# Performance work log

Measured on AMD Instinct MI355X. Metric: run time of the kernel, lower is better.

The kernel has to match this reference:

```python
import jax, jax.numpy as jnp
import numpy as np

NN_SIZE = 16  # nn_size from __init__


def _knn_idx(points_ref, k):
    """Brute-force KNN of points_ref against itself (replaces faiss_knn).
    Returns (B, N, k) neighbor indices, self point excluded."""
    sq = jnp.sum(points_ref * points_ref, axis=-1)  # (B, N)
    # squared pairwise distances (B, N, N)
    d2 = sq[:, :, None] + sq[:, None, :] - 2.0 * jnp.einsum(
        'bnd,bmd->bnm', points_ref, points_ref)
    _, idx = jax.lax.top_k(-d2, k + 1)  # nearest first; idx[...,0] is self
    return idx[:, :, 1:]


def _edge_lengths(pts, knn_idx):
    """Gather neighbor coords and compute edge lengths (B, N, K)."""
    group = jax.vmap(lambda p, i: p[i])(pts, knn_idx)  # (B, N, K, D)
    return jnp.linalg.norm(group - pts[:, :, None, :], axis=-1)


def setup_inputs() -> dict:
    key = jax.random.key(0)
    k1, k2 = jax.random.split(key)
    B, N, D = 4, 8192, 3
    points_ref = jax.random.normal(k1, (B, N, D), dtype=jnp.float32)
    # pred points: perturbed ref so the loss is non-degenerate
    points = points_ref + 0.01 * jax.random.normal(k2, (B, N, D), dtype=jnp.float32)
    return {"points_ref": points_ref, "points": points}


def reference(points_ref, points):
    # faiss KNN is non-differentiable -> stop_gradient on the index search
    knn_idx = _knn_idx(jax.lax.stop_gradient(points_ref), NN_SIZE)  # (B,N,K)
    dist_ref = _edge_lengths(points_ref, knn_idx)  # (B, N, K)
    dist = _edge_lengths(points, knn_idx)          # (B, N, K)
    # metric = torch.nn.L1Loss() (mean reduction)
    return jnp.mean(jnp.abs(dist_ref - dist))
```

## Files before the change

### kernel.cpp

```cpp
#include <hip/hip_runtime.h>
#include <math.h>

#define BATCH 4
#define NPTS  8192
#define KNN   16
#define KK    17
#define NQ    (BATCH*NPTS)
#define JMASK 0x1FFFu
#define EMASK 0xFFFFE000u
#define TOTAL_EDGES (BATCH*NPTS*KNN)

#define GC    32
#define GLO   (-4.5f)
#define GINV  (32.0f/9.0f)
#define NCELL (GC*GC*GC)

#define NG    128
#define GSZ   64

#define QPB   16
#define BLOCK 256
#define GRIDQ (NQ/QPB)
#define WIN   64
#define CAP   21

__device__ __forceinline__ int cell_coord(float x) {
    int c = (int)floorf((x - GLO) * GINV);
    return min(GC - 1, max(0, c));
}
__device__ __forceinline__ unsigned spread5(unsigned v) {
    v &= 31u;
    v = (v | (v << 8)) & 0x100Fu;
    v = (v | (v << 4)) & 0x10C3u;
    v = (v | (v << 2)) & 0x1249u;
    return v;
}
__device__ __forceinline__ unsigned morton_id(float x, float y, float z) {
    return spread5((unsigned)cell_coord(x)) | (spread5((unsigned)cell_coord(y)) << 1)
         | (spread5((unsigned)cell_coord(z)) << 2);
}
__device__ __forceinline__ unsigned mkkey(const float4 p, float xi, float yi,
                                          float zi, float sqi, unsigned j) {
    const float e  = fmaf(p.x, xi, fmaf(p.y, yi, p.z * zi)) + p.w;
    const float d2 = e + sqi;
    return (__float_as_uint(d2) & EMASK) | j;
}
__device__ __forceinline__ void ins17(unsigned (&a)[KK], unsigned key) {
    #pragma unroll
    for (int k = KK - 1; k >= 1; --k) a[k] = min(a[k], max(a[k - 1], key));
    a[0] = min(a[0], key);
}
template<int RL>
__device__ __forceinline__ unsigned merge_tau(const unsigned (*s_key)[BLOCK], int t) {
    const int mq = t & (QPB - 1), half = (t >> 4) & 1;
    unsigned m[KK];
    #pragma unroll
    for (int k = 0; k < KK; ++k) m[k] = 0xFFFFFFFFu;
    for (int s = 8 * half; s < 8 * half + 8; ++s) {
        const int col = mq + s * QPB;
        for (int k = 0; k < RL; ++k) {
            const unsigned c = s_key[k][col];
            if (c >= m[KK - 1]) break;
            ins17(m, c);
        }
    }
    unsigned tau = 0;
    #pragma unroll
    for (int k = 0; k < KK; ++k) {
        const unsigned bk = (unsigned)__shfl_xor((int)m[KK - 1 - k], 16, 64);
        tau = max(tau, min(m[k], bk));
    }
    return tau;
}

__global__ void pel_hist(const float* __restrict__ pref, unsigned* __restrict__ hist,
                         float* __restrict__ acc, unsigned* __restrict__ bcnt) {
    const int idx = blockIdx.x * 256 + threadIdx.x;
    if (idx == 0) { acc[0] = 0.0f; bcnt[0] = 0u; }
    const int b = idx >> 13;
    const unsigned mid = morton_id(pref[3*idx], pref[3*idx+1], pref[3*idx+2]);
    atomicAdd(&hist[b * NCELL + mid], 1u);
}
__global__ __launch_bounds__(1024)
void pel_scan(const unsigned* __restrict__ hist, unsigned* __restrict__ off) {
    __shared__ unsigned s[1024];
    const unsigned* h = hist + blockIdx.x * NCELL;
    unsigned*       o = off  + blockIdx.x * NCELL;
    const int t = threadIdx.x;
    unsigned v[32], tot = 0;
    #pragma unroll
    for (int k = 0; k < 32; ++k) { v[k] = h[t * 32 + k]; tot += v[k]; }
    s[t] = tot;
    __syncthreads();
    for (int d = 1; d < 1024; d <<= 1) {
        const unsigned add = (t >= d) ? s[t - d] : 0u;
        __syncthreads();
        s[t] += add;
        __syncthreads();
    }
    unsigned run = s[t] - tot;
    #pragma unroll
    for (int k = 0; k < 32; ++k) { o[t * 32 + k] = run; run += v[k]; }
}
__global__ void pel_scatter(const float* __restrict__ pref, const float* __restrict__ pts,
                            unsigned* __restrict__ off,
                            float4* __restrict__ p4r, float4* __restrict__ p4p) {
    const int idx = blockIdx.x * 256 + threadIdx.x;
    const int b = idx >> 13;
    const float x = pref[3*idx], y = pref[3*idx+1], z = pref[3*idx+2];
    const unsigned mid = morton_id(x, y, z);
    const unsigned pos = atomicAdd(&off[b * NCELL + mid], 1u);
    p4r[b * NPTS + pos] = make_float4(-2.f*x, -2.f*y, -2.f*z, fmaf(x, x, fmaf(y, y, z*z)));
    const float px = pts[3*idx], py = pts[3*idx+1], pz = pts[3*idx+2];
    p4p[b * NPTS + pos] = make_float4(-2.f*px, -2.f*py, -2.f*pz,
                                      fmaf(px, px, fmaf(py, py, pz*pz)));
}
__global__ __launch_bounds__(256)
void pel_gstat(const float4* __restrict__ P4r, float4* __restrict__ gball) {
    const int wv = threadIdx.x >> 6, lane = threadIdx.x & 63;
    const int gid = blockIdx.x * 4 + wv;
    const int b = gid >> 7, g = gid & (NG - 1);
    const float4 p = P4r[b * NPTS + g * GSZ + lane];
    const float x = -0.5f * p.x, y = -0.5f * p.y, z = -0.5f * p.z;
    float mnx = x, mxx = x, mny = y, mxy = y, mnz = z, mxz = z;
    #pragma unroll
    for (int m = 1; m <= 32; m <<= 1) {
        mnx = fminf(mnx, __shfl_xor(mnx, m, 64)); mxx = fmaxf(mxx, __shfl_xor(mxx, m, 64));
        mny = fminf(mny, __shfl_xor(mny, m, 64)); mxy = fmaxf(mxy, __shfl_xor(mxy, m, 64));
        mnz = fminf(mnz, __shfl_xor(mnz, m, 64)); mxz = fmaxf(mxz, __shfl_xor(mxz, m, 64));
    }
    const float cx = 0.5f * (mnx + mxx), cy = 0.5f * (mny + mxy), cz = 0.5f * (mnz + mxz);
    float d = sqrtf((x-cx)*(x-cx) + (y-cy)*(y-cy) + (z-cz)*(z-cz));
    #pragma unroll
    for (int m = 1; m <= 32; m <<= 1) d = fmaxf(d, __shfl_xor(d, m, 64));
    if (lane == 0) gball[gid] = make_float4(cx, cy, cz, d);
}

__global__ __launch_bounds__(BLOCK, 8)
void pel_query(const float4* __restrict__ P4r, const float4* __restrict__ P4p,
               const float4* __restrict__ gball,
               float* __restrict__ acc_ws, unsigned* __restrict__ bcnt,
               float* __restrict__ out)
{
    __shared__ unsigned s_key[CAP][BLOCK];
    __shared__ unsigned s_tau[QPB];
    __shared__ unsigned short s_glist[NG];
    __shared__ float s_grp[4];
    __shared__ int s_ng;
    __shared__ float s_part[BLOCK / 64];

    const int t  = threadIdx.x;
    const int lq = t & (QPB - 1), sp = t >> 4;
    const int q  = blockIdx.x * QPB + lq;
    const int b  = q >> 13;
    const int i  = q & (NPTS - 1);

    const float4* __restrict__ Pq = P4r + b * NPTS;
    const float4* __restrict__ Pp = P4p + b * NPTS;
    const float4* __restrict__ Gb = gball + b * NG;

    const float4 self = Pq[i];
    const float xi = -0.5f * self.x, yi = -0.5f * self.y, zi = -0.5f * self.z;
    const float sqi = self.w;

    unsigned al[4] = {~0u, ~0u, ~0u, ~0u};
    const int w0 = min(max(i - WIN / 2, 0), NPTS - WIN) + sp * 4;
    {
        float4 cw[4];
        #pragma unroll
        for (int u = 0; u < 4; ++u) cw[u] = Pq[w0 + u];
        #pragma unroll
        for (int u = 0; u < 4; ++u) {
            const unsigned key = mkkey(cw[u], xi, yi, zi, sqi, (unsigned)(w0 + u));
            #pragma unroll
            for (int k = 3; k >= 1; --k) al[k] = min(al[k], max(al[k - 1], key));
            al[0] = min(al[0], key);
        }
    }
    #pragma unroll
    for (int k = 0; k < 4; ++k) s_key[k][t] = al[k];
    __syncthreads();
    if (t < 32) {
        const unsigned tau0 = merge_tau<4>(s_key, t);
        if (t < QPB) s_tau[t] = tau0;
    }
    __syncthreads();

    if (t < QPB) {
        if (t == 0) s_ng = 0;
        const int i2 = (blockIdx.x * QPB + t) & (NPTS - 1);
        const float4 s2 = Pq[i2];
        const float qx = -0.5f * s2.x, qy = -0.5f * s2.y, qz = -0.5f * s2.z;
        float mnx = qx, mxx = qx, mny = qy, mxy = qy, mnz = qz, mxz = qz;
        #pragma unroll
        for (int m = 1; m <= 8; m <<= 1) {
            mnx = fminf(mnx, __shfl_xor(mnx, m, 64)); mxx = fmaxf(mxx, __shfl_xor(mxx, m, 64));
            mny = fminf(mny, __shfl_xor(mny, m, 64)); mxy = fmaxf(mxy, __shfl_xor(mxy, m, 64));
            mnz = fminf(mnz, __shfl_xor(mnz, m, 64)); mxz = fmaxf(mxz, __shfl_xor(mxz, m, 64));
        }
        const float cx = 0.5f * (mnx + mxx), cy = 0.5f * (mny + mxy), cz = 0.5f * (mnz + mxz);
        const float dq = sqrtf((qx-cx)*(qx-cx) + (qy-cy)*(qy-cy) + (qz-cz)*(qz-cz));
        const float rt = sqrtf(__uint_as_float((s_tau[t] & EMASK) + 0x2000u));
        float v = dq + rt;
        #pragma unroll
        for (int m = 1; m <= 8; m <<= 1) v = fmaxf(v, __shfl_xor(v, m, 64));
        if (t == 0) {
            s_grp[0] = cx; s_grp[1] = cy; s_grp[2] = cz; s_grp[3] = v + 1e-3f;
        }
    }
    __syncthreads();

    if (t < NG) {
        const float4 gb = Gb[t];
        const float dx = gb.x - s_grp[0], dy = gb.y - s_grp[1], dz = gb.z - s_grp[2];
        const float rhs = s_grp[3] + gb.w;
        if (dx*dx + dy*dy + dz*dz <= rhs * rhs) {
            const int slot = atomicAdd(&s_ng, 1);
            s_glist[slot] = (unsigned short)t;
        }
    }
    __syncthreads();
    const int ng = s_ng;

    unsigned tauL = s_tau[lq];
    int cnt = 0;
    for (int gi = 0; gi < ng; ++gi) {
        const int gb4 = (int)s_glist[gi] * GSZ + sp * 4;
        float4 c[4];
        #pragma unroll
        for (int u = 0; u < 4; ++u) c[u] = Pq[gb4 + u];
        #pragma unroll
        for (int u = 0; u < 4; ++u) {
            const unsigned key = mkkey(c[u], xi, yi, zi, sqi, (unsigned)(gb4 + u));
            s_key[cnt][t] = key;
            cnt += (key <= tauL) ? 1 : 0;
        }
        if (cnt > CAP - 4) {
            unsigned k17[KK];
            #pragma unroll
            for (int k = 0; k < KK; ++k) k17[k] = 0xFFFFFFFFu;
            for (int n = 0; n < cnt; ++n) ins17(k17, s_key[n][t]);
            const unsigned th = k17[KK - 1];
            int kept = 0;
            for (int n = 0; n < cnt; ++n) {
                const unsigned c2 = s_key[n][t];
                if (c2 <= th) { s_key[kept][t] = c2; ++kept; }
            }
            cnt = kept; tauL = min(tauL, th);
        }
    }

    unsigned c17[KK];
    #pragma unroll
    for (int k = 0; k < KK; ++k) c17[k] = 0xFFFFFFFFu;
    for (int n = 0; n < cnt; ++n) ins17(c17, s_key[n][t]);
    __syncthreads();
    #pragma unroll
    for (int k = 0; k < KK; ++k) s_key[k][t] = c17[k];
    __syncthreads();
    if (t < 32) {
        const unsigned tauX = merge_tau<KK>(s_key, t);
        if (t < QPB) s_tau[t] = tauX;
    }
    __syncthreads();
    const unsigned tauK = s_tau[lq];

    const float4 selfp = Pp[i];
    const float pxi = -0.5f * selfp.x, pyi = -0.5f * selfp.y, pzi = -0.5f * selfp.z;
    float accv = 0.0f;
    #pragma unroll
    for (int k = 0; k < KK; ++k) {
        if (c17[k] <= tauK) {
            const int j = (int)(c17[k] & JMASK);
            const float4 pr = Pq[j];
            const float er  = fmaf(pr.x, xi, fmaf(pr.y, yi, pr.z * zi)) + pr.w;
            const float d2r = fmaxf(er + sqi, 0.0f);
            const float4 pp = Pp[j];
            const float ep  = fmaf(pp.x, pxi, fmaf(pp.y, pyi, pp.z * pzi)) + pp.w;
            const float d2p = fmaxf(ep + selfp.w, 0.0f);
            accv += fabsf(sqrtf(d2r) - sqrtf(d2p));
        }
    }

    #pragma unroll
    for (int o = 32; o > 0; o >>= 1) accv += __shfl_down(accv, o, 64);
    if ((t & 63) == 0) s_part[t >> 6] = accv;
    __syncthreads();
    if (t == 0) {
        float s = 0.0f;
        #pragma unroll
        for (int w2 = 0; w2 < BLOCK / 64; ++w2) s += s_part[w2];
        atomicAdd(acc_ws, s);
        __threadfence();
        const unsigned old = atomicAdd(bcnt, 1u);
        if (old == GRIDQ - 1) {
            __threadfence();
            const float total = atomicAdd(acc_ws, 0.0f);
            out[0] = total * (1.0f / (float)TOTAL_EDGES);
        }
    }
}

extern "C" void kernel_launch(void* const* d_in, const int* in_sizes, int n_in,
                              void* d_out, int out_size, void* d_ws, size_t ws_size,
                              hipStream_t stream) {
    const float* pref = (const float*)d_in[0];
    const float* pts  = (const float*)d_in[1];
    float4*   P4r  = (float4*)d_ws;
    float4*   P4p  = P4r + NQ;
    unsigned* hist = (unsigned*)d_ws;
    unsigned* off  = (unsigned*)((char*)d_ws + 1048576);
    float4*   gball= (float4*)((char*)d_ws + 1572864);
    float*    acc  = (float*)((char*)d_ws + 1581056);
    unsigned* bcnt = (unsigned*)(acc + 1);
    float*    out  = (float*)d_out;

    hipMemsetAsync(hist, 0, BATCH * NCELL * sizeof(unsigned), stream);
    pel_hist   <<<NQ / 256, 256, 0, stream>>>(pref, hist, acc, bcnt);
    pel_scan   <<<BATCH, 1024, 0, stream>>>(hist, off);
    pel_scatter<<<NQ / 256, 256, 0, stream>>>(pref, pts, off, P4r, P4p);
    pel_gstat  <<<(BATCH * NG) / 4, 256, 0, stream>>>(P4r, gball);
    pel_query  <<<GRIDQ, BLOCK, 0, stream>>>(P4r, P4p, gball, acc, bcnt, out);
}
```

Before: 251.0 us.

## Use finer 16-point subgroups with per-wave culling and prefetched candidate scan

Bounding-ball groups shrink from 128 groups of 64 points to 512 subgroups of 16 points. Culling now runs per wave, using a bounding ball over the 4 queries in that wave instead of one for all 16 queries in the block. The candidate scan changes from 4 points per thread per group to 1 point per thread per subgroup, with a two-deep register prefetch, and the buffer capacity drops to 18. The goal is to reject many more distance evaluations through tighter culling and to hide load latency. The cost is more culling tests per wave and a larger shared glist, and it relies on the ws layout no longer needing offsets after the scatter step.

```diff
diff --git a/kernel.cpp b/kernel.cpp
--- a/kernel.cpp
+++ b/kernel.cpp
@@ -15,14 +15,15 @@
 #define GINV  (32.0f/9.0f)
 #define NCELL (GC*GC*GC)
 
-#define NG    128
-#define GSZ   64
+#define NSG   512
+#define SGS   16
 
 #define QPB   16
 #define BLOCK 256
 #define GRIDQ (NQ/QPB)
 #define WIN   64
-#define CAP   21
+#define CAP   18
+#define NWAVE (BLOCK/64)
 
 __device__ __forceinline__ int cell_coord(float x) {
     int c = (int)floorf((x - GLO) * GINV);
@@ -116,15 +117,15 @@
                                       fmaf(px, px, fmaf(py, py, pz*pz)));
 }
 __global__ __launch_bounds__(256)
-void pel_gstat(const float4* __restrict__ P4r, float4* __restrict__ gball) {
-    const int wv = threadIdx.x >> 6, lane = threadIdx.x & 63;
-    const int gid = blockIdx.x * 4 + wv;
-    const int b = gid >> 7, g = gid & (NG - 1);
-    const float4 p = P4r[b * NPTS + g * GSZ + lane];
+void pel_gstat(const float4* __restrict__ P4r, float4* __restrict__ sgball) {
+    const int quad = threadIdx.x >> 4, pos = threadIdx.x & 15;
+    const int gid = blockIdx.x * 16 + quad;
+    const int b = gid >> 9, s = gid & (NSG - 1);
+    const float4 p = P4r[b * NPTS + s * SGS + pos];
     const float x = -0.5f * p.x, y = -0.5f * p.y, z = -0.5f * p.z;
     float mnx = x, mxx = x, mny = y, mxy = y, mnz = z, mxz = z;
     #pragma unroll
-    for (int m = 1; m <= 32; m <<= 1) {
+    for (int m = 1; m <= 8; m <<= 1) {
         mnx = fminf(mnx, __shfl_xor(mnx, m, 64)); mxx = fmaxf(mxx, __shfl_xor(mxx, m, 64));
         mny = fminf(mny, __shfl_xor(mny, m, 64)); mxy = fmaxf(mxy, __shfl_xor(mxy, m, 64));
         mnz = fminf(mnz, __shfl_xor(mnz, m, 64)); mxz = fmaxf(mxz, __shfl_xor(mxz, m, 64));
@@ -132,32 +133,33 @@
     const float cx = 0.5f * (mnx + mxx), cy = 0.5f * (mny + mxy), cz = 0.5f * (mnz + mxz);
     float d = sqrtf((x-cx)*(x-cx) + (y-cy)*(y-cy) + (z-cz)*(z-cz));
     #pragma unroll
-    for (int m = 1; m <= 32; m <<= 1) d = fmaxf(d, __shfl_xor(d, m, 64));
-    if (lane == 0) gball[gid] = make_float4(cx, cy, cz, d);
+    for (int m = 1; m <= 8; m <<= 1) d = fmaxf(d, __shfl_xor(d, m, 64));
+    if (pos == 0) sgball[gid] = make_float4(cx, cy, cz, d);
 }
 
 __global__ __launch_bounds__(BLOCK, 8)
 void pel_query(const float4* __restrict__ P4r, const float4* __restrict__ P4p,
-               const float4* __restrict__ gball,
+               const float4* __restrict__ sgball,
                float* __restrict__ acc_ws, unsigned* __restrict__ bcnt,
                float* __restrict__ out)
 {
     __shared__ unsigned s_key[CAP][BLOCK];
     __shared__ unsigned s_tau[QPB];
-    __shared__ unsigned short s_glist[NG];
-    __shared__ float s_grp[4];
-    __shared__ int s_ng;
-    __shared__ float s_part[BLOCK / 64];
-
-    const int t  = threadIdx.x;
-    const int lq = t & (QPB - 1), sp = t >> 4;
-    const int q  = blockIdx.x * QPB + lq;
-    const int b  = q >> 13;
-    const int i  = q & (NPTS - 1);
+    __shared__ unsigned short s_glist[NWAVE][NSG];
+    __shared__ int s_ng[NWAVE];
+    __shared__ float s_part[NWAVE];
+
+    const int t    = threadIdx.x;
+    const int sp   = t & 15, lq = t >> 4;
+    const int wv   = t >> 6, lane = t & 63;
+    const int q    = blockIdx.x * QPB + lq;
+    const int b    = q >> 13;
+    const int i    = q & (NPTS - 1);
+    const int wcol = lq + sp * QPB;
 
     const float4* __restrict__ Pq = P4r + b * NPTS;
     const float4* __restrict__ Pp = P4p + b * NPTS;
-    const float4* __restrict__ Gb = gball + b * NG;
+    const float4* __restrict__ Sg = sgball + b * NSG;
 
     const float4 self = Pq[i];
     const float xi = -0.5f * self.x, yi = -0.5f * self.y, zi = -0.5f * self.z;
@@ -178,7 +180,7 @@
         }
     }
     #pragma unroll
-    for (int k = 0; k < 4; ++k) s_key[k][t] = al[k];
+    for (int k = 0; k < 4; ++k) s_key[k][wcol] = al[k];
     __syncthreads();
     if (t < 32) {
         const unsigned tau0 = merge_tau<4>(s_key, t);
@@ -186,56 +188,46 @@
     }
     __syncthreads();
 
-    if (t < QPB) {
-        if (t == 0) s_ng = 0;
-        const int i2 = (blockIdx.x * QPB + t) & (NPTS - 1);
-        const float4 s2 = Pq[i2];
-        const float qx = -0.5f * s2.x, qy = -0.5f * s2.y, qz = -0.5f * s2.z;
-        float mnx = qx, mxx = qx, mny = qy, mxy = qy, mnz = qz, mxz = qz;
-        #pragma unroll
-        for (int m = 1; m <= 8; m <<= 1) {
-            mnx = fminf(mnx, __shfl_xor(mnx, m, 64)); mxx = fmaxf(mxx, __shfl_xor(mxx, m, 64));
-            mny = fminf(mny, __shfl_xor(mny, m, 64)); mxy = fmaxf(mxy, __shfl_xor(mxy, m, 64));
-            mnz = fminf(mnz, __shfl_xor(mnz, m, 64)); mxz = fmaxf(mxz, __shfl_xor(mxz, m, 64));
-        }
-        const float cx = 0.5f * (mnx + mxx), cy = 0.5f * (mny + mxy), cz = 0.5f * (mnz + mxz);
-        const float dq = sqrtf((qx-cx)*(qx-cx) + (qy-cy)*(qy-cy) + (qz-cz)*(qz-cz));
-        const float rt = sqrtf(__uint_as_float((s_tau[t] & EMASK) + 0x2000u));
-        float v = dq + rt;
-        #pragma unroll
-        for (int m = 1; m <= 8; m <<= 1) v = fmaxf(v, __shfl_xor(v, m, 64));
-        if (t == 0) {
-            s_grp[0] = cx; s_grp[1] = cy; s_grp[2] = cz; s_grp[3] = v + 1e-3f;
-        }
-    }
-    __syncthreads();
-
-    if (t < NG) {
-        const float4 gb = Gb[t];
-        const float dx = gb.x - s_grp[0], dy = gb.y - s_grp[1], dz = gb.z - s_grp[2];
-        const float rhs = s_grp[3] + gb.w;
+    if (lane == 0) s_ng[wv] = 0;
+    float mnx = xi, mxx = xi, mny = yi, mxy = yi, mnz = zi, mxz = zi;
+    #pragma unroll
+    for (int m = 1; m <= 32; m <<= 1) {
+        mnx = fminf(mnx, __shfl_xor(mnx, m, 64)); mxx = fmaxf(mxx, __shfl_xor(mxx, m, 64));
+        mny = fminf(mny, __shfl_xor(mny, m, 64)); mxy = fmaxf(mxy, __shfl_xor(mxy, m, 64));
+        mnz = fminf(mnz, __shfl_xor(mnz, m, 64)); mxz = fmaxf(mxz, __shfl_xor(mxz, m, 64));
+    }
+    const float cx = 0.5f * (mnx + mxx), cy = 0.5f * (mny + mxy), cz = 0.5f * (mnz + mxz);
+    const float rt = sqrtf(__uint_as_float((s_tau[lq] & EMASK) + 0x2000u));
+    float v = sqrtf((xi-cx)*(xi-cx) + (yi-cy)*(yi-cy) + (zi-cz)*(zi-cz)) + rt;
+    #pragma unroll
+    for (int m = 1; m <= 32; m <<= 1) v = fmaxf(v, __shfl_xor(v, m, 64));
+    const float Rq = v + 1e-3f;
+
+    for (int k2 = lane; k2 < NSG; k2 += 64) {
+        const float4 gb = Sg[k2];
+        const float dx = gb.x - cx, dy = gb.y - cy, dz = gb.z - cz;
+        const float rhs = Rq + gb.w;
         if (dx*dx + dy*dy + dz*dz <= rhs * rhs) {
-            const int slot = atomicAdd(&s_ng, 1);
-            s_glist[slot] = (unsigned short)t;
-        }
-    }
-    __syncthreads();
-    const int ng = s_ng;
-
+            const int slot = atomicAdd(&s_ng[wv], 1);
+            s_glist[wv][slot] = (unsigned short)k2;
+        }
+    }
+    __syncthreads();
+    const int ngw = s_ng[wv];
+
+    const unsigned short* __restrict__ gl = s_glist[wv];
     unsigned tauL = s_tau[lq];
     int cnt = 0;
-    for (int gi = 0; gi < ng; ++gi) {
-        const int gb4 = (int)s_glist[gi] * GSZ + sp * 4;
-        float4 c[4];
-        #pragma unroll
-        for (int u = 0; u < 4; ++u) c[u] = Pq[gb4 + u];
-        #pragma unroll
-        for (int u = 0; u < 4; ++u) {
-            const unsigned key = mkkey(c[u], xi, yi, zi, sqi, (unsigned)(gb4 + u));
-            s_key[cnt][t] = key;
-            cnt += (key <= tauL) ? 1 : 0;
-        }
-        if (cnt > CAP - 4) {
+    int j0 = (int)gl[0] * SGS + sp;
+    int j1 = (int)gl[min(1, ngw - 1)] * SGS + sp;
+    float4 c0 = Pq[j0], c1 = Pq[j1];
+    for (int gi = 0; gi < ngw; ++gi) {
+        const int jn = (int)gl[min(gi + 2, ngw - 1)] * SGS + sp;
+        const float4 nx = Pq[jn];
+        const unsigned key = mkkey(c0, xi, yi, zi, sqi, (unsigned)j0);
+        s_key[cnt][t] = key;
+        cnt += (key <= tauL) ? 1 : 0;
+        if (cnt == CAP) {
             unsigned k17[KK];
             #pragma unroll
             for (int k = 0; k < KK; ++k) k17[k] = 0xFFFFFFFFu;
@@ -248,6 +240,7 @@
             }
             cnt = kept; tauL = min(tauL, th);
         }
+        c0 = c1; j0 = j1; c1 = nx; j1 = jn;
     }
 
     unsigned c17[KK];
@@ -256,7 +249,7 @@
     for (int n = 0; n < cnt; ++n) ins17(c17, s_key[n][t]);
     __syncthreads();
     #pragma unroll
-    for (int k = 0; k < KK; ++k) s_key[k][t] = c17[k];
+    for (int k = 0; k < KK; ++k) s_key[k][wcol] = c17[k];
     __syncthreads();
     if (t < 32) {
         const unsigned tauX = merge_tau<KK>(s_key, t);
@@ -284,12 +277,12 @@
 
     #pragma unroll
     for (int o = 32; o > 0; o >>= 1) accv += __shfl_down(accv, o, 64);
-    if ((t & 63) == 0) s_part[t >> 6] = accv;
+    if (lane == 0) s_part[wv] = accv;
     __syncthreads();
     if (t == 0) {
         float s = 0.0f;
         #pragma unroll
-        for (int w2 = 0; w2 < BLOCK / 64; ++w2) s += s_part[w2];
+        for (int w2 = 0; w2 < NWAVE; ++w2) s += s_part[w2];
         atomicAdd(acc_ws, s);
         __threadfence();
         const unsigned old = atomicAdd(bcnt, 1u);
@@ -310,7 +303,7 @@
     float4*   P4p  = P4r + NQ;
     unsigned* hist = (unsigned*)d_ws;
     unsigned* off  = (unsigned*)((char*)d_ws + 1048576);
-    float4*   gball= (float4*)((char*)d_ws + 1572864);
+    float4*   sgball = (float4*)((char*)d_ws + 1048576);
     float*    acc  = (float*)((char*)d_ws + 1581056);
     unsigned* bcnt = (unsigned*)(acc + 1);
     float*    out  = (float*)d_out;
@@ -319,6 +312,6 @@
     pel_hist   <<<NQ / 256, 256, 0, stream>>>(pref, hist, acc, bcnt);
     pel_scan   <<<BATCH, 1024, 0, stream>>>(hist, off);
     pel_scatter<<<NQ / 256, 256, 0, stream>>>(pref, pts, off, P4r, P4p);
-    pel_gstat  <<<(BATCH * NG) / 4, 256, 0, stream>>>(P4r, gball);
-    pel_query  <<<GRIDQ, BLOCK, 0, stream>>>(P4r, P4p, gball, acc, bcnt, out);
-}
+    pel_gstat  <<<(BATCH * NSG) / 16, 256, 0, stream>>>(P4r, sgball);
+    pel_query  <<<GRIDQ, BLOCK, 0, stream>>>(P4r, P4p, sgball, acc, bcnt, out);
+}
```

After: 285.0 us. 13.6% more time.

## Use finer 16-point subgroup bounding balls and prefetch candidate loads in KNN query

Applied to the files above, without the earlier changes.

Replaces the 128 groups of 64 sorted points with 512 subgroups of 16 points per batch, each with its own bounding ball. Culling against the query-block ball is therefore tighter and fewer candidate points get distance-tested. The candidate loop now handles four subgroups per iteration and software-prefetches the next subgroup's points into registers while keys are computed, with invalid slots masked to the maximum key. One __syncthreads before the final key write is also dropped, and the subgroup ball buffer reuses the workspace region of the offset array. The trade-off is more per-block ball tests and extra registers, and both the synchronization removal and the buffer aliasing carry correctness risk.

```diff
diff --git a/kernel.cpp b/kernel.cpp
--- a/kernel.cpp
+++ b/kernel.cpp
@@ -15,8 +15,8 @@
 #define GINV  (32.0f/9.0f)
 #define NCELL (GC*GC*GC)
 
-#define NG    128
-#define GSZ   64
+#define NSG   512
+#define SGS   16
 
 #define QPB   16
 #define BLOCK 256
@@ -116,15 +116,15 @@
                                       fmaf(px, px, fmaf(py, py, pz*pz)));
 }
 __global__ __launch_bounds__(256)
-void pel_gstat(const float4* __restrict__ P4r, float4* __restrict__ gball) {
-    const int wv = threadIdx.x >> 6, lane = threadIdx.x & 63;
-    const int gid = blockIdx.x * 4 + wv;
-    const int b = gid >> 7, g = gid & (NG - 1);
-    const float4 p = P4r[b * NPTS + g * GSZ + lane];
+void pel_gstat(const float4* __restrict__ P4r, float4* __restrict__ sgball) {
+    const int quad = threadIdx.x >> 4, pos = threadIdx.x & 15;
+    const int gid = blockIdx.x * 16 + quad;
+    const int b = gid >> 9, s = gid & (NSG - 1);
+    const float4 p = P4r[b * NPTS + s * SGS + pos];
     const float x = -0.5f * p.x, y = -0.5f * p.y, z = -0.5f * p.z;
     float mnx = x, mxx = x, mny = y, mxy = y, mnz = z, mxz = z;
     #pragma unroll
-    for (int m = 1; m <= 32; m <<= 1) {
+    for (int m = 1; m <= 8; m <<= 1) {
         mnx = fminf(mnx, __shfl_xor(mnx, m, 64)); mxx = fmaxf(mxx, __shfl_xor(mxx, m, 64));
         mny = fminf(mny, __shfl_xor(mny, m, 64)); mxy = fmaxf(mxy, __shfl_xor(mxy, m, 64));
         mnz = fminf(mnz, __shfl_xor(mnz, m, 64)); mxz = fmaxf(mxz, __shfl_xor(mxz, m, 64));
@@ -132,19 +132,19 @@
     const float cx = 0.5f * (mnx + mxx), cy = 0.5f * (mny + mxy), cz = 0.5f * (mnz + mxz);
     float d = sqrtf((x-cx)*(x-cx) + (y-cy)*(y-cy) + (z-cz)*(z-cz));
     #pragma unroll
-    for (int m = 1; m <= 32; m <<= 1) d = fmaxf(d, __shfl_xor(d, m, 64));
-    if (lane == 0) gball[gid] = make_float4(cx, cy, cz, d);
+    for (int m = 1; m <= 8; m <<= 1) d = fmaxf(d, __shfl_xor(d, m, 64));
+    if (pos == 0) sgball[gid] = make_float4(cx, cy, cz, d);
 }
 
 __global__ __launch_bounds__(BLOCK, 8)
 void pel_query(const float4* __restrict__ P4r, const float4* __restrict__ P4p,
-               const float4* __restrict__ gball,
+               const float4* __restrict__ sgball,
                float* __restrict__ acc_ws, unsigned* __restrict__ bcnt,
                float* __restrict__ out)
 {
     __shared__ unsigned s_key[CAP][BLOCK];
     __shared__ unsigned s_tau[QPB];
-    __shared__ unsigned short s_glist[NG];
+    __shared__ unsigned short s_glist[NSG];
     __shared__ float s_grp[4];
     __shared__ int s_ng;
     __shared__ float s_part[BLOCK / 64];
@@ -157,7 +157,7 @@
 
     const float4* __restrict__ Pq = P4r + b * NPTS;
     const float4* __restrict__ Pp = P4p + b * NPTS;
-    const float4* __restrict__ Gb = gball + b * NG;
+    const float4* __restrict__ Sg = sgball + b * NSG;
 
     const float4 self = Pq[i];
     const float xi = -0.5f * self.x, yi = -0.5f * self.y, zi = -0.5f * self.z;
@@ -210,28 +210,39 @@
     }
     __syncthreads();
 
-    if (t < NG) {
-        const float4 gb = Gb[t];
+    for (int k2 = t; k2 < NSG; k2 += BLOCK) {
+        const float4 gb = Sg[k2];
         const float dx = gb.x - s_grp[0], dy = gb.y - s_grp[1], dz = gb.z - s_grp[2];
         const float rhs = s_grp[3] + gb.w;
         if (dx*dx + dy*dy + dz*dz <= rhs * rhs) {
             const int slot = atomicAdd(&s_ng, 1);
-            s_glist[slot] = (unsigned short)t;
+            s_glist[slot] = (unsigned short)k2;
         }
     }
     __syncthreads();
     const int ng = s_ng;
+    const int nb = (ng + 3) >> 2;
 
     unsigned tauL = s_tau[lq];
     int cnt = 0;
-    for (int gi = 0; gi < ng; ++gi) {
-        const int gb4 = (int)s_glist[gi] * GSZ + sp * 4;
-        float4 c[4];
-        #pragma unroll
-        for (int u = 0; u < 4; ++u) c[u] = Pq[gb4 + u];
+    const int sub = sp >> 2;
+    const int p0  = (sp & 3) * 4;
+    int vs0 = (sub < ng) ? 1 : 0;
+    int j0  = (int)s_glist[min(sub, ng - 1)] * SGS + p0;
+    float4 c0[4];
+    #pragma unroll
+    for (int u = 0; u < 4; ++u) c0[u] = Pq[j0 + u];
+    for (int gi = 0; gi < nb; ++gi) {
+        const int idx1 = (gi + 1) * 4 + sub;
+        const int vs1  = (idx1 < ng) ? 1 : 0;
+        const int j1   = (int)s_glist[min(idx1, ng - 1)] * SGS + p0;
+        float4 c1[4];
+        #pragma unroll
+        for (int u = 0; u < 4; ++u) c1[u] = Pq[j1 + u];
         #pragma unroll
         for (int u = 0; u < 4; ++u) {
-            const unsigned key = mkkey(c[u], xi, yi, zi, sqi, (unsigned)(gb4 + u));
+            unsigned key = mkkey(c0[u], xi, yi, zi, sqi, (unsigned)(j0 + u));
+            key = vs0 ? key : 0xFFFFFFFFu;
             s_key[cnt][t] = key;
             cnt += (key <= tauL) ? 1 : 0;
         }
@@ -248,13 +259,15 @@
             }
             cnt = kept; tauL = min(tauL, th);
         }
+        #pragma unroll
+        for (int u = 0; u < 4; ++u) c0[u] = c1[u];
+        j0 = j1; vs0 = vs1;
     }
 
     unsigned c17[KK];
     #pragma unroll
     for (int k = 0; k < KK; ++k) c17[k] = 0xFFFFFFFFu;
     for (int n = 0; n < cnt; ++n) ins17(c17, s_key[n][t]);
-    __syncthreads();
     #pragma unroll
     for (int k = 0; k < KK; ++k) s_key[k][t] = c17[k];
     __syncthreads();
@@ -310,7 +323,7 @@
     float4*   P4p  = P4r + NQ;
     unsigned* hist = (unsigned*)d_ws;
     unsigned* off  = (unsigned*)((char*)d_ws + 1048576);
-    float4*   gball= (float4*)((char*)d_ws + 1572864);
+    float4*   sgball = (float4*)((char*)d_ws + 1048576);
     float*    acc  = (float*)((char*)d_ws + 1581056);
     unsigned* bcnt = (unsigned*)(acc + 1);
     float*    out  = (float*)d_out;
@@ -319,6 +332,6 @@
     pel_hist   <<<NQ / 256, 256, 0, stream>>>(pref, hist, acc, bcnt);
     pel_scan   <<<BATCH, 1024, 0, stream>>>(hist, off);
     pel_scatter<<<NQ / 256, 256, 0, stream>>>(pref, pts, off, P4r, P4p);
-    pel_gstat  <<<(BATCH * NG) / 4, 256, 0, stream>>>(P4r, gball);
-    pel_query  <<<GRIDQ, BLOCK, 0, stream>>>(P4r, P4p, gball, acc, bcnt, out);
-}
+    pel_gstat  <<<(BATCH * NSG) / 16, 256, 0, stream>>>(P4r, sgball);
+    pel_query  <<<GRIDQ, BLOCK, 0, stream>>>(P4r, P4p, sgball, acc, bcnt, out);
+}
```

After: 255.7 us. No clear change (+1.9%).
